# Optimization experiments

Hardware: AMD Instinct MI355X
Metric: run time of the kernel (lower is better)

## Reference

```python
import jax, jax.numpy as jnp
import numpy as np

B, T, D = 4, 1024, 1024
N_HEAD, HEAD, LATENT = 16, 64, 32
N_EXP, TOP_K, N_FF = 8, 2, 4096
HID = int(2 * N_FF / 3)  # 2730, Expert hidden when ffn_multiplier is None
CAP_FACTOR = 1.0


def setup_inputs() -> dict:
    key = jax.random.key(0)
    ks = jax.random.split(key, 14)
    s = 0.02
    f = lambda k, shp: jax.random.normal(k, shp, jnp.float32) * s
    return dict(
        x=jax.random.normal(ks[0], (B, T, D), jnp.float32),
        noise_eps=jax.random.normal(ks[1], (B, T, N_EXP), jnp.float32),
        ln1_w=jnp.ones((D,), jnp.float32),
        ln2_w=jnp.ones((D,), jnp.float32),
        q_w=f(ks[2], (N_HEAD, D, HEAD)), q_b=jnp.zeros((N_HEAD, HEAD), jnp.float32),
        ka_w=f(ks[3], (N_HEAD, D, LATENT)), kb_w=f(ks[4], (N_HEAD, LATENT, HEAD)),
        va_w=f(ks[5], (N_HEAD, D, LATENT)), vb_w=f(ks[6], (N_HEAD, LATENT, HEAD)),
        proj_w=f(ks[7], (D, D)), proj_b=jnp.zeros((D,), jnp.float32),
        route_w=f(ks[8], (D, N_EXP)), route_b=jnp.zeros((N_EXP,), jnp.float32),
        noise_w=f(ks[9], (D, N_EXP)), noise_b=jnp.zeros((N_EXP,), jnp.float32),
        swiglu_w=f(ks[10], (N_EXP, D, 2 * HID)),
        down_w=f(ks[11], (N_EXP, HID, D)),
    )


def _rms(x, w, eps=1e-5):
    x32 = x.astype(jnp.float32)
    n = x32 * jax.lax.rsqrt(jnp.mean(x32 * x32, -1, keepdims=True) + eps)
    return n.astype(x.dtype) * w


def _rope(q, k):
    # q,k: [B,H,T,hd]; even/odd split then concatenated halves (matches torch code)
    hd, Tq = q.shape[-1], q.shape[-2]
    inv = 1.0 / (10000.0 ** (jnp.arange(0, hd, 2, dtype=jnp.float32) / hd))
    ang = jnp.arange(Tq, dtype=jnp.float32)[:, None] * inv[None, :]  # [T, hd/2]
    cos, sin = jnp.cos(ang), jnp.sin(ang)
    def rot(t):
        t1, t2 = t[..., ::2], t[..., 1::2]
        return jnp.concatenate([t1 * cos - t2 * sin, t1 * sin + t2 * cos], -1)
    return rot(q), rot(k)


def reference(x, noise_eps, ln1_w, ln2_w, q_w, q_b, ka_w, kb_w, va_w, vb_w,
              proj_w, proj_b, route_w, route_b, noise_w, noise_b, swiglu_w, down_w):
    Bx, Tx, Dm = x.shape
    hd = q_w.shape[-1]
    E = route_w.shape[-1]
    # ---- Multi-Head Latent Attention (pre-norm) ----
    xn = _rms(x, ln1_w)
    q = jnp.einsum('btd,hde->bhte', xn, q_w) + q_b[None, :, None, :]
    k = jnp.einsum('bhtl,hle->bhte', jnp.einsum('btd,hdl->bhtl', xn, ka_w), kb_w)
    v = jnp.einsum('bhtl,hle->bhte', jnp.einsum('btd,hdl->bhtl', xn, va_w), vb_w)
    q, k = _rope(q, k)
    scores = jnp.einsum('bhtd,bhsd->bhts', q, k) / jnp.sqrt(jnp.float32(hd))
    attn = jax.nn.softmax(scores, axis=-1)  # NOTE: no causal mask in source
    o = jnp.einsum('bhts,bhsd->bhtd', attn, v)
    o = o.transpose(0, 2, 1, 3).reshape(Bx, Tx, Dm)
    x = x + (o @ proj_w + proj_b)
    # ---- Noisy top-k router ----
    xn2 = _rms(x, ln2_w)
    logits = xn2 @ route_w + route_b
    noisy = logits + noise_eps * jax.nn.softplus(xn2 @ noise_w + noise_b)  # temperature=1
    _, topi = jax.lax.top_k(noisy, TOP_K)  # [B,T,k]
    sel = jnp.any(jax.nn.one_hot(topi, E, dtype=jnp.bool_), axis=-2)  # [B,T,E]
    probs = jax.nn.softmax(jnp.where(sel, noisy, -jnp.inf), axis=-1)
    aux = jnp.sum((jnp.mean(probs, (0, 1)) - 1.0 / E) ** 2)
    # ---- Capacity-limited expert dispatch (first-come in flat token order) ----
    N = Bx * Tx
    cap = int(N * TOP_K / E * CAP_FACTOR)
    flat_x = xn2.reshape(N, Dm)
    flat_p = probs.reshape(N, E)
    flat_i = topi.reshape(N, TOP_K)
    upd = jnp.zeros((N, Dm), x.dtype)
    for e in range(E):
        m = jnp.any(flat_i == e, axis=-1)            # [N]
        pos = jnp.cumsum(m) - 1                      # slot within expert buffer
        keep = m & (pos < cap)
        slot = jnp.where(keep, pos, cap)             # dropped -> overflow slot
        tok = jnp.zeros(cap + 1, jnp.int32).at[slot].set(jnp.arange(N, dtype=jnp.int32))[:cap]
        valid = jnp.zeros(cap + 1, jnp.bool_).at[slot].set(keep)[:cap]
        xe = flat_x[tok] * valid[:, None]            # [cap, D]; zero rows yield zero output (no biases)
        h = xe @ swiglu_w[e]
        h1, h2 = jnp.split(h, 2, axis=-1)
        oe = (jax.nn.silu(h1) * h2) @ down_w[e]
        gate = jnp.where(valid, flat_p[tok, e], 0.0)
        upd = upd.at[tok].add(oe * gate[:, None])
    return x + upd.reshape(Bx, Tx, Dm), aux
```

## Files before the change

### kernel.cpp

```cpp
#include <hip/hip_runtime.h>
#include <math.h>

#define NTOK   4096
#define DM     1024
#define NHEAD  16
#define HDIM   64
#define NEXP   8
#define CAP    1024
#define HID    2730
#define NFF2   5460
#define HIDP   2752
#define KCD    86

typedef __attribute__((ext_vector_type(8))) short bf16x8;
typedef __attribute__((ext_vector_type(4))) float f32x4;
typedef __attribute__((ext_vector_type(8))) _Float16 h16x8;
typedef __attribute__((ext_vector_type(4))) _Float16 h16x4;
typedef __attribute__((ext_vector_type(8))) unsigned short u16x8;

__device__ __forceinline__ unsigned short f2bf(float f) {
  unsigned int u = __float_as_uint(f);
  u += 0x7fffu + ((u >> 16) & 1u);
  return (unsigned short)(u >> 16);
}

__global__ __launch_bounds__(256) void pack_dense3(const float* __restrict__ q_w,
                                                   const float* __restrict__ ka_w,
                                                   const float* __restrict__ va_w,
                                                   const float* __restrict__ proj_w,
                                                   unsigned short* __restrict__ Wqt,
                                                   unsigned short* __restrict__ Wlatt,
                                                   unsigned short* __restrict__ Wprojt) {
  int b = blockIdx.x;
  int tid = threadIdx.x;
  int col = tid & 63;
  int k0 = (tid >> 6) * 8;
  int which = b >> 9;
  int bb = b & 511;
  int nt = bb >> 5, kc = bb & 31;
  int d0 = kc * 32 + k0;
  u16x8 o;
  if (which == 0) {
    const float* src = q_w + ((size_t)nt * 1024 + d0) * 64 + col;
#pragma unroll
    for (int j = 0; j < 8; j++) o[j] = f2bf(src[(size_t)j * 64]);
    *(u16x8*)(Wqt + (size_t)bb * 2048 + col * 32 + k0) = o;
  } else if (which == 1) {
    int n = nt * 64 + col;
    const float* base;
    int h, l;
    if (n < 512) { h = n >> 5; l = n & 31; base = ka_w; }
    else { int m = n - 512; h = m >> 5; l = m & 31; base = va_w; }
    const float* src = base + ((size_t)h * 1024 + d0) * 32 + l;
#pragma unroll
    for (int j = 0; j < 8; j++) o[j] = f2bf(src[(size_t)j * 32]);
    *(u16x8*)(Wlatt + (size_t)bb * 2048 + col * 32 + k0) = o;
  } else {
    int n = nt * 64 + col;
    const float* src = proj_w + (size_t)d0 * 1024 + n;
#pragma unroll
    for (int j = 0; j < 8; j++) o[j] = f2bf(src[(size_t)j * 1024]);
    *(u16x8*)(Wprojt + (size_t)bb * 2048 + col * 32 + k0) = o;
  }
}

__global__ __launch_bounds__(256) void pack_swiglu(const float* __restrict__ swiglu_w,
                                                   unsigned short* __restrict__ Wpk) {
  int b = blockIdx.x;
  int kc32 = b & 31;
  int ejt = b >> 5;
  int jt = ejt % 43;
  int e = ejt / 43;
  int tid = threadIdx.x;
  int col = tid & 63;
  int k0 = (tid >> 6) * 8;
  int n = jt * 64 + col;
  bool nv = n < HID;
  const float* src = swiglu_w + ((size_t)e * DM + kc32 * 32 + k0) * NFF2 + n;
  u16x8 o1, o2;
#pragma unroll
  for (int j = 0; j < 8; j++) {
    float v1 = nv ? src[(size_t)j * NFF2] : 0.f;
    float v2 = nv ? src[(size_t)j * NFF2 + HID] : 0.f;
    o1[j] = f2bf(v1);
    o2[j] = f2bf(v2);
  }
  unsigned short* dst = Wpk + (size_t)b * 4096 + col * 32 + k0;
  *(u16x8*)dst = o1;
  *(u16x8*)(dst + 2048) = o2;
}

__global__ __launch_bounds__(256) void pack_down(const float* __restrict__ down_w,
                                                 unsigned short* __restrict__ Wdk) {
  int b = blockIdx.x;
  int kci = b % KCD;
  int ent = b / KCD;
  int nt = ent & 15;
  int e = ent >> 4;
  int tid = threadIdx.x;
  int col = tid & 63, k0 = (tid >> 6) * 8;
  int n = nt * 64 + col;
  int kbase = kci * 32 + k0;
  const float* src = down_w + ((size_t)e * HID + kbase) * DM + n;
  u16x8 o;
#pragma unroll
  for (int j = 0; j < 8; j++) {
    float v = (kbase + j < HID) ? src[(size_t)j * DM] : 0.f;
    o[j] = f2bf(v);
  }
  *(u16x8*)(Wdk + (size_t)b * 2048 + col * 32 + k0) = o;
}

template <bool F32OUT>
__global__ __launch_bounds__(256) void rms_kernel(const float* __restrict__ x,
                                                  const float* __restrict__ w,
                                                  float* __restrict__ out,
                                                  unsigned short* __restrict__ outb) {
  int row = blockIdx.x;
  int tid = threadIdx.x;
  const float4 v = ((const float4*)(x + (size_t)row * DM))[tid];
  float ss = v.x * v.x + v.y * v.y + v.z * v.z + v.w * v.w;
#pragma unroll
  for (int off = 32; off >= 1; off >>= 1) ss += __shfl_down(ss, off);
  __shared__ float red[4];
  if ((tid & 63) == 0) red[tid >> 6] = ss;
  __syncthreads();
  float tot = red[0] + red[1] + red[2] + red[3];
  float scale = rsqrtf(tot * (1.0f / 1024.0f) + 1e-5f);
  const float4 wv = ((const float4*)w)[tid];
  float4 o;
  o.x = v.x * scale * wv.x; o.y = v.y * scale * wv.y;
  o.z = v.z * scale * wv.z; o.w = v.w * scale * wv.w;
  if (F32OUT) ((float4*)(out + (size_t)row * DM))[tid] = o;
  ushort4 ob;
  ob.x = f2bf(o.x); ob.y = f2bf(o.y); ob.z = f2bf(o.z); ob.w = f2bf(o.w);
  *(ushort4*)(outb + (size_t)row * DM + tid * 4) = ob;
}

template <bool BIAS, bool RES>
__global__ __launch_bounds__(256) void mfma_dense(const unsigned short* __restrict__ A,
                                                  const unsigned short* __restrict__ Bpk,
                                                  const float* __restrict__ bias,
                                                  const float* __restrict__ res,
                                                  float* __restrict__ C, int K, int N) {
  int m0 = blockIdx.x * 128;
  int n0 = blockIdx.y * 128;
  int KC = K >> 5;
  __shared__ short As[128][40];
  __shared__ short Bs[128][40];
  int tid = threadIdx.x;
  int wid = tid >> 6, lane = tid & 63;
  int wm0 = (wid >> 1) * 64, wn0 = (wid & 1) * 64;
  int lr = lane & 15, lq = lane >> 4;
  f32x4 c[4][4];
  f32x4 zz = {0.f, 0.f, 0.f, 0.f};
#pragma unroll
  for (int i = 0; i < 4; i++)
#pragma unroll
    for (int j = 0; j < 4; j++) c[i][j] = zz;
  int ar = tid >> 2, aq = tid & 3;
  const unsigned short* Ap0 = A + (size_t)(m0 + ar) * K + aq * 8;
  const unsigned short* Ap1 = A + (size_t)(m0 + 64 + ar) * K + aq * 8;
  const unsigned short* Bt = Bpk + (size_t)(n0 >> 6) * KC * 2048 + tid * 8;
  u16x8 ra0 = *(const u16x8*)Ap0;
  u16x8 ra1 = *(const u16x8*)Ap1;
  u16x8 rb0 = *(const u16x8*)Bt;
  u16x8 rb1 = *(const u16x8*)(Bt + (size_t)KC * 2048);
  for (int kci = 0; kci < KC; kci++) {
    __syncthreads();
    *(u16x8*)&As[ar][aq * 8] = ra0;
    *(u16x8*)&As[64 + ar][aq * 8] = ra1;
    *(u16x8*)&Bs[tid >> 2][(tid & 3) * 8] = rb0;
    *(u16x8*)&Bs[64 + (tid >> 2)][(tid & 3) * 8] = rb1;
    __syncthreads();
    if (kci + 1 < KC) {
      ra0 = *(const u16x8*)(Ap0 + (kci + 1) * 32);
      ra1 = *(const u16x8*)(Ap1 + (kci + 1) * 32);
      rb0 = *(const u16x8*)(Bt + (size_t)(kci + 1) * 2048);
      rb1 = *(const u16x8*)(Bt + (size_t)(KC + kci + 1) * 2048);
    }
    bf16x8 a[4], b[4];
#pragma unroll
    for (int mi = 0; mi < 4; mi++) a[mi] = *(bf16x8*)&As[wm0 + mi * 16 + lr][lq * 8];
#pragma unroll
    for (int ni = 0; ni < 4; ni++) b[ni] = *(bf16x8*)&Bs[wn0 + ni * 16 + lr][lq * 8];
#pragma unroll
    for (int mi = 0; mi < 4; mi++)
#pragma unroll
      for (int ni = 0; ni < 4; ni++)
        c[mi][ni] = __builtin_amdgcn_mfma_f32_16x16x32_bf16(a[mi], b[ni], c[mi][ni], 0, 0, 0);
  }
#pragma unroll
  for (int mi = 0; mi < 4; mi++)
#pragma unroll
    for (int ni = 0; ni < 4; ni++) {
      int nn = n0 + wn0 + ni * 16 + lr;
      float bv = BIAS ? bias[nn] : 0.f;
#pragma unroll
      for (int r = 0; r < 4; r++) {
        int mm = m0 + wm0 + mi * 16 + lq * 4 + r;
        float v = c[mi][ni][r] + bv;
        if (RES) v += res[(size_t)mm * N + nn];
        C[(size_t)mm * N + nn] = v;
      }
    }
}

__global__ void expand_kernel(const float* __restrict__ latents, const float* __restrict__ kb_w,
                              const float* __restrict__ vb_w, float* __restrict__ kpre,
                              _Float16* __restrict__ vf) {
  int idx = blockIdx.x * 256 + threadIdx.x;
  int e = idx & 63;
  int t = (idx >> 6) & 1023;
  int h = (idx >> 16) & 15;
  int b = idx >> 20;
  const float* lrow = latents + ((size_t)(b * 1024 + t)) * DM;
  const float* kb = kb_w + (size_t)h * 2048;
  const float* vb = vb_w + (size_t)h * 2048;
  float ka = 0.f, va = 0.f;
#pragma unroll
  for (int l = 0; l < 32; l++) {
    ka += lrow[h * 32 + l] * kb[l * 64 + e];
    va += lrow[512 + h * 32 + l] * vb[l * 64 + e];
  }
  kpre[idx] = ka;
  vf[idx] = (_Float16)va;
}

template <bool IN_BTHD>
__global__ void rope_kernel(const float* __restrict__ in, _Float16* __restrict__ out) {
  int idx = blockIdx.x * 256 + threadIdx.x;
  int i = idx & 31;
  int t = (idx >> 5) & 1023;
  int h = (idx >> 15) & 15;
  int b = idx >> 19;
  size_t ib;
  if (IN_BTHD)
    ib = ((size_t)(b * 1024 + t)) * DM + h * 64;
  else
    ib = ((size_t)((b * 16 + h) * 1024 + t)) * 64;
  float t1 = in[ib + 2 * i], t2 = in[ib + 2 * i + 1];
  float inv = exp2f(-(float)i * 0.41524101186091903f);
  float ang = (float)t * inv;
  float s, c;
  sincosf(ang, &s, &c);
  size_t ob = ((size_t)((b * 16 + h) * 1024 + t)) * 64;
  out[ob + i] = (_Float16)(t1 * c - t2 * s);
  out[ob + 32 + i] = (_Float16)(t1 * s + t2 * c);
}

__global__ __launch_bounds__(256) void attn_mfma(const _Float16* __restrict__ qf,
                                                 const _Float16* __restrict__ kf,
                                                 const _Float16* __restrict__ vf,
                                                 unsigned short* __restrict__ o) {
  __shared__ _Float16 Ks[64][72];
  __shared__ _Float16 Vt[64][68];
  int bh = blockIdx.y;
  int q0 = blockIdx.x * 64;
  int tid = threadIdx.x;
  int wv = tid >> 6, lane = tid & 63;
  int lr = lane & 15, lq = lane >> 4;
  const size_t base = (size_t)bh * 1024 * 64;
  const _Float16* qrow = qf + base + (size_t)(q0 + wv * 16 + lr) * 64;
  h16x8 qfr[2];
  qfr[0] = *(const h16x8*)(qrow + lq * 8);
  qfr[1] = *(const h16x8*)(qrow + 32 + lq * 8);
  float mrow = -3.0e38f, lsum = 0.f;
  f32x4 oacc[4];
  f32x4 zz = {0.f, 0.f, 0.f, 0.f};
#pragma unroll
  for (int i = 0; i < 4; i++) oacc[i] = zz;
  int skey = tid >> 2, spart = tid & 3;
  int vkey = tid & 63, vdb = (tid >> 6) * 16;

// ... 95 lines not shown
    const float* nw = noise_w + d * 8;
#pragma unroll
    for (int e = 0; e < 8; e++) {
      acc[e] += xv * rw[e];
      nacc[e] += xv * nw[e];
    }
  }
#pragma unroll
  for (int off = 32; off >= 1; off >>= 1) {
#pragma unroll
    for (int e = 0; e < 8; e++) {
      acc[e] += __shfl_down(acc[e], off);
      nacc[e] += __shfl_down(nacc[e], off);
    }
  }
  if (lane == 0) {
    float noisy[8];
#pragma unroll
    for (int e = 0; e < 8; e++) {
      float lg = acc[e] + route_b[e];
      float nl = nacc[e] + noise_b[e];
      float sp = (nl > 20.f) ? nl : log1pf(expf(nl));
      noisy[e] = lg + noise_eps[tk * 8 + e] * sp;
    }
    int i1 = 0;
    float n1 = noisy[0];
#pragma unroll
    for (int e = 1; e < 8; e++)
      if (noisy[e] > n1) { n1 = noisy[e]; i1 = e; }
    int i2 = -1;
    float n2 = -3.0e38f;
#pragma unroll
    for (int e = 0; e < 8; e++)
      if (e != i1 && noisy[e] > n2) { n2 = noisy[e]; i2 = e; }
    float r = expf(n2 - n1);
    float p1 = 1.0f / (1.0f + r);
    float p2 = r / (1.0f + r);
    topi[tk * 2] = i1;
    topi[tk * 2 + 1] = i2;
#pragma unroll
    for (int e = 0; e < 8; e++) flat_p[tk * 8 + e] = (e == i1) ? p1 : ((e == i2) ? p2 : 0.f);
    atomicAdd(&probsum[i1], p1);
    atomicAdd(&probsum[i2], p2);
    slotmap[tk * 2] = -1;
    slotmap[tk * 2 + 1] = -1;
  }
}

__global__ __launch_bounds__(512) void scan_kernel(const int* __restrict__ topi,
                                                   const float* __restrict__ flat_p,
                                                   int* __restrict__ tok, float* __restrict__ gate,
                                                   int* __restrict__ cnt, int* __restrict__ slotmap) {
  int e = threadIdx.x >> 6;
  int lane = threadIdx.x & 63;
  int count = 0;
  for (int base = 0; base < NTOK; base += 64) {
    int t = base + lane;
    int a = topi[t * 2], b = topi[t * 2 + 1];
    bool mflag = (a == e) || (b == e);
    unsigned long long mask = __ballot(mflag);
    int pos = count + __popcll(mask & ((1ull << lane) - 1ull));
    if (mflag && pos < CAP) {
      tok[e * CAP + pos] = t;
      gate[e * CAP + pos] = flat_p[t * 8 + e];
      int k = (a == e) ? 0 : 1;
      slotmap[t * 2 + k] = pos;
    }
    count += __popcll(mask);
  }
  if (lane == 0) cnt[e] = (count < CAP) ? count : CAP;
}

__global__ __launch_bounds__(256) void mfma_swiglu(const unsigned short* __restrict__ xn2b,
                                                   const unsigned short* __restrict__ Wpk,
                                                   const int* __restrict__ tok,
                                                   const int* __restrict__ cnt,
                                                   unsigned short* __restrict__ ACT) {
  int L = blockIdx.x;
  int e = L & 7;
  int gw = L >> 3;
  int m0 = (gw & 7) * 128;
  int jt = gw >> 3;
  int j0 = jt * 64;
  __shared__ short As[128][40];
  __shared__ short B1s[64][40];
  __shared__ short B2s[64][40];
  __shared__ int tokL[128];
  int tid = threadIdx.x;
  if (tid < 128) {
    int slot = m0 + tid;
    tokL[tid] = (slot < cnt[e]) ? tok[e * CAP + slot] : 0;
  }
  __syncthreads();
  int wid = tid >> 6, lane = tid & 63;
  int wm0 = (wid >> 1) * 64, wn0 = (wid & 1) * 32;
  int lr = lane & 15, lq = lane >> 4;
  f32x4 c1[4][2], c2[4][2];
  f32x4 zz = {0.f, 0.f, 0.f, 0.f};
#pragma unroll
  for (int i = 0; i < 4; i++)
#pragma unroll
    for (int j = 0; j < 2; j++) { c1[i][j] = zz; c2[i][j] = zz; }
  int ar = tid >> 2, aq = tid & 3;
  const unsigned short* Ap0 = xn2b + (size_t)tokL[ar] * DM + aq * 8;
  const unsigned short* Ap1 = xn2b + (size_t)tokL[64 + ar] * DM + aq * 8;
  const unsigned short* wp = Wpk + (size_t)(e * 43 + jt) * 32 * 4096 + tid * 8;
  u16x8 ra0 = *(const u16x8*)Ap0;
  u16x8 ra1 = *(const u16x8*)Ap1;
  u16x8 rb1 = *(const u16x8*)wp;
  u16x8 rb2 = *(const u16x8*)(wp + 2048);

  for (int kci = 0; kci < 32; kci++) {
    __syncthreads();
    *(u16x8*)&As[ar][aq * 8] = ra0;
    *(u16x8*)&As[64 + ar][aq * 8] = ra1;
    *(u16x8*)&B1s[tid >> 2][(tid & 3) * 8] = rb1;
    *(u16x8*)&B2s[tid >> 2][(tid & 3) * 8] = rb2;
    __syncthreads();
    if (kci < 31) {
      ra0 = *(const u16x8*)(Ap0 + (kci + 1) * 32);
      ra1 = *(const u16x8*)(Ap1 + (kci + 1) * 32);
      rb1 = *(const u16x8*)(wp + (size_t)(kci + 1) * 4096);
      rb2 = *(const u16x8*)(wp + (size_t)(kci + 1) * 4096 + 2048);
    }
    bf16x8 a[4], b1[2], b2[2];
#pragma unroll
    for (int mi = 0; mi < 4; mi++) a[mi] = *(bf16x8*)&As[wm0 + mi * 16 + lr][lq * 8];
#pragma unroll
    for (int ni = 0; ni < 2; ni++) {
      b1[ni] = *(bf16x8*)&B1s[wn0 + ni * 16 + lr][lq * 8];
      b2[ni] = *(bf16x8*)&B2s[wn0 + ni * 16 + lr][lq * 8];
    }
#pragma unroll
    for (int mi = 0; mi < 4; mi++)
#pragma unroll
      for (int ni = 0; ni < 2; ni++) {
        c1[mi][ni] = __builtin_amdgcn_mfma_f32_16x16x32_bf16(a[mi], b1[ni], c1[mi][ni], 0, 0, 0);
        c2[mi][ni] = __builtin_amdgcn_mfma_f32_16x16x32_bf16(a[mi], b2[ni], c2[mi][ni], 0, 0, 0);
      }
  }
#pragma unroll
  for (int mi = 0; mi < 4; mi++)
#pragma unroll
    for (int ni = 0; ni < 2; ni++)
#pragma unroll
      for (int r = 0; r < 4; r++) {
        int mm = m0 + wm0 + mi * 16 + lq * 4 + r;
        int cc = j0 + wn0 + ni * 16 + lr;
        float h1 = c1[mi][ni][r], h2 = c2[mi][ni][r];
        float act = (h1 / (1.0f + expf(-h1))) * h2;
        ACT[(size_t)e * CAP * HIDP + (size_t)mm * HIDP + cc] = f2bf(act);
      }
}

__global__ __launch_bounds__(256) void mfma_down(const unsigned short* __restrict__ ACT,
                                                 const unsigned short* __restrict__ Wdk,
                                                 float* __restrict__ OE) {
  int L = blockIdx.x;
  int e = L & 7;
  int gw = L >> 3;
  int m0 = (gw & 7) * 128;
  int nt0 = (gw >> 3) * 2;
  int n0 = nt0 * 64;
  __shared__ short As[128][40];
  __shared__ short Bs[128][40];
  int tid = threadIdx.x;
  int wid = tid >> 6, lane = tid & 63;
  int wm0 = (wid >> 1) * 64, wn0 = (wid & 1) * 64;
  int lr = lane & 15, lq = lane >> 4;
  f32x4 c[4][4];
  f32x4 zz = {0.f, 0.f, 0.f, 0.f};
#pragma unroll
  for (int i = 0; i < 4; i++)
#pragma unroll
    for (int j = 0; j < 4; j++) c[i][j] = zz;
  int ar = tid >> 2, aq = tid & 3;
  const unsigned short* Ab = ACT + (size_t)e * CAP * HIDP + (size_t)m0 * HIDP;
  const unsigned short* Ap0 = Ab + (size_t)ar * HIDP + aq * 8;
  const unsigned short* Ap1 = Ab + (size_t)(64 + ar) * HIDP + aq * 8;
  const unsigned short* Bt = Wdk + (size_t)(e * 16 + nt0) * KCD * 2048 + tid * 8;
  u16x8 ra0 = *(const u16x8*)Ap0;
  u16x8 ra1 = *(const u16x8*)Ap1;
  u16x8 rb0 = *(const u16x8*)Bt;
  u16x8 rb1 = *(const u16x8*)(Bt + (size_t)KCD * 2048);

  for (int kci = 0; kci < KCD; kci++) {
    __syncthreads();
    *(u16x8*)&As[ar][aq * 8] = ra0;
    *(u16x8*)&As[64 + ar][aq * 8] = ra1;
    *(u16x8*)&Bs[tid >> 2][(tid & 3) * 8] = rb0;
    *(u16x8*)&Bs[64 + (tid >> 2)][(tid & 3) * 8] = rb1;
    __syncthreads();
    if (kci + 1 < KCD) {
      ra0 = *(const u16x8*)(Ap0 + (kci + 1) * 32);
      ra1 = *(const u16x8*)(Ap1 + (kci + 1) * 32);
      rb0 = *(const u16x8*)(Bt + (size_t)(kci + 1) * 2048);
      rb1 = *(const u16x8*)(Bt + (size_t)(KCD + kci + 1) * 2048);
    }
    bf16x8 a[4], b[4];
#pragma unroll
    for (int mi = 0; mi < 4; mi++) a[mi] = *(bf16x8*)&As[wm0 + mi * 16 + lr][lq * 8];
#pragma unroll
    for (int ni = 0; ni < 4; ni++) b[ni] = *(bf16x8*)&Bs[wn0 + ni * 16 + lr][lq * 8];
#pragma unroll
    for (int mi = 0; mi < 4; mi++)
#pragma unroll
      for (int ni = 0; ni < 4; ni++)
        c[mi][ni] = __builtin_amdgcn_mfma_f32_16x16x32_bf16(a[mi], b[ni], c[mi][ni], 0, 0, 0);
  }
#pragma unroll
  for (int mi = 0; mi < 4; mi++)
#pragma unroll
    for (int ni = 0; ni < 4; ni++)
#pragma unroll
      for (int r = 0; r < 4; r++) {
        int mm = m0 + wm0 + mi * 16 + lq * 4 + r;
        int nn = n0 + wn0 + ni * 16 + lr;
        OE[((size_t)e << 20) + (size_t)mm * DM + nn] = c[mi][ni][r];
      }
}

__global__ void combine_kernel(const float* __restrict__ x2, const float* __restrict__ OE,
                               const int* __restrict__ topi, const int* __restrict__ slotmap,
                               const float* __restrict__ flat_p, float* __restrict__ out) {
  int idx = blockIdx.x * 256 + threadIdx.x;
  int t = idx >> 8;
  int c4 = (idx & 255) * 4;
  float4 v = *(const float4*)(x2 + (size_t)t * DM + c4);
#pragma unroll
  for (int k = 0; k < 2; k++) {
    int s = slotmap[t * 2 + k];
    if (s >= 0) {
      int e = topi[t * 2 + k];
      float g = flat_p[t * 8 + e];
      float4 ov = *(const float4*)(OE + ((size_t)e << 20) + (size_t)s * DM + c4);
      v.x += g * ov.x; v.y += g * ov.y; v.z += g * ov.z; v.w += g * ov.w;
    }
  }
  *(float4*)(out + (size_t)t * DM + c4) = v;
}

__global__ void aux_kernel(const float* __restrict__ probsum, float* __restrict__ out) {
  if (threadIdx.x == 0) {
    float s = 0.f;
#pragma unroll
    for (int e = 0; e < 8; e++) {
      float d = probsum[e] * (1.0f / 4096.0f) - 0.125f;
      s += d * d;
    }
    out[4194304] = s;
  }
}

extern "C" void kernel_launch(void* const* d_in, const int* in_sizes, int n_in, void* d_out,
                              int out_size, void* d_ws, size_t ws_size, hipStream_t stream) {
  const float* x = (const float*)d_in[0];
  const float* noise_eps = (const float*)d_in[1];
  const float* ln1_w = (const float*)d_in[2];
  const float* ln2_w = (const float*)d_in[3];
  const float* q_w = (const float*)d_in[4];
  const float* q_b = (const float*)d_in[5];
  const float* ka_w = (const float*)d_in[6];
  const float* kb_w = (const float*)d_in[7];
  const float* va_w = (const float*)d_in[8];
  const float* vb_w = (const float*)d_in[9];
  const float* proj_w = (const float*)d_in[10];
  const float* proj_b = (const float*)d_in[11];
  const float* route_w = (const float*)d_in[12];
  const float* route_b = (const float*)d_in[13];
  const float* noise_w = (const float*)d_in[14];
  const float* noise_b = (const float*)d_in[15];
  const float* swiglu_w = (const float*)d_in[16];
  const float* down_w = (const float*)d_in[17];
  float* out = (float*)d_out;
  char* w = (char*)d_ws;
  const size_t MB = 1ull << 20;

  float* x2 = (float*)(w + 0 * MB);
  float* xn2 = (float*)(w + 16 * MB);
  unsigned short* xn2b = (unsigned short*)(w + 32 * MB);
  char* sm = w + 40 * MB;
  unsigned short* xnb = (unsigned short*)(w + 42 * MB);
  float* qtmp = (float*)(w + 50 * MB);
  float* latents = (float*)(w + 66 * MB);
  float* kpre = (float*)(w + 82 * MB);
  _Float16* qfb = (_Float16*)(w + 98 * MB);
  _Float16* kfb = (_Float16*)(w + 106 * MB);
  _Float16* vfb = (_Float16*)(w + 114 * MB);
  unsigned short* obb = (unsigned short*)(w + 122 * MB);
  unsigned short* Wqt = (unsigned short*)(w + 130 * MB);
  unsigned short* Wlatt = (unsigned short*)(w + 132 * MB);
  unsigned short* Wprojt = (unsigned short*)(w + 134 * MB);
// ... 35 lines not shown
```

Before: 942.3 us.

## Process two K-chunks per barrier and remap weight pack/LDS store layout

Measured after the change: 923.3 us. -2.0%, faster.

```diff
diff --git a/kernel.cpp b/kernel.cpp
--- a/kernel.cpp
+++ b/kernel.cpp
@@ -44,7 +44,7 @@
     const float* src = q_w + ((size_t)nt * 1024 + d0) * 64 + col;
 #pragma unroll
     for (int j = 0; j < 8; j++) o[j] = f2bf(src[(size_t)j * 64]);
-    *(u16x8*)(Wqt + (size_t)bb * 2048 + col * 32 + k0) = o;
+    *(u16x8*)(Wqt + (size_t)bb * 2048 + tid * 8) = o;
   } else if (which == 1) {
     int n = nt * 64 + col;
     const float* base;
@@ -54,13 +54,13 @@
     const float* src = base + ((size_t)h * 1024 + d0) * 32 + l;
 #pragma unroll
     for (int j = 0; j < 8; j++) o[j] = f2bf(src[(size_t)j * 32]);
-    *(u16x8*)(Wlatt + (size_t)bb * 2048 + col * 32 + k0) = o;
+    *(u16x8*)(Wlatt + (size_t)bb * 2048 + tid * 8) = o;
   } else {
     int n = nt * 64 + col;
     const float* src = proj_w + (size_t)d0 * 1024 + n;
 #pragma unroll
     for (int j = 0; j < 8; j++) o[j] = f2bf(src[(size_t)j * 1024]);
-    *(u16x8*)(Wprojt + (size_t)bb * 2048 + col * 32 + k0) = o;
+    *(u16x8*)(Wprojt + (size_t)bb * 2048 + tid * 8) = o;
   }
 }
 
@@ -85,7 +85,7 @@
     o1[j] = f2bf(v1);
     o2[j] = f2bf(v2);
   }
-  unsigned short* dst = Wpk + (size_t)b * 4096 + col * 32 + k0;
+  unsigned short* dst = Wpk + (size_t)b * 4096 + tid * 8;
   *(u16x8*)dst = o1;
   *(u16x8*)(dst + 2048) = o2;
 }
@@ -108,7 +108,7 @@
     float v = (kbase + j < HID) ? src[(size_t)j * DM] : 0.f;
     o[j] = f2bf(v);
   }
-  *(u16x8*)(Wdk + (size_t)b * 2048 + col * 32 + k0) = o;
+  *(u16x8*)(Wdk + (size_t)b * 2048 + tid * 8) = o;
 }
 
 template <bool F32OUT>
@@ -146,50 +146,61 @@
   int m0 = blockIdx.x * 128;
   int n0 = blockIdx.y * 128;
   int KC = K >> 5;
-  __shared__ short As[128][40];
-  __shared__ short Bs[128][40];
+  int KK = KC >> 1;
+  __shared__ short As[2][128][40];
+  __shared__ short Bs[2][128][40];
   int tid = threadIdx.x;
-  int wid = tid >> 6, lane = tid & 63;
+  int l6 = tid & 63, wid = tid >> 6;
+  int lr = l6 & 15, lq = l6 >> 4;
   int wm0 = (wid >> 1) * 64, wn0 = (wid & 1) * 64;
-  int lr = lane & 15, lq = lane >> 4;
   f32x4 c[4][4];
   f32x4 zz = {0.f, 0.f, 0.f, 0.f};
 #pragma unroll
   for (int i = 0; i < 4; i++)
 #pragma unroll
     for (int j = 0; j < 4; j++) c[i][j] = zz;
-  int ar = tid >> 2, aq = tid & 3;
-  const unsigned short* Ap0 = A + (size_t)(m0 + ar) * K + aq * 8;
-  const unsigned short* Ap1 = A + (size_t)(m0 + 64 + ar) * K + aq * 8;
+  const unsigned short* Ap0 = A + (size_t)(m0 + l6) * K + wid * 8;
+  const unsigned short* Ap1 = A + (size_t)(m0 + 64 + l6) * K + wid * 8;
   const unsigned short* Bt = Bpk + (size_t)(n0 >> 6) * KC * 2048 + tid * 8;
-  u16x8 ra0 = *(const u16x8*)Ap0;
-  u16x8 ra1 = *(const u16x8*)Ap1;
-  u16x8 rb0 = *(const u16x8*)Bt;
-  u16x8 rb1 = *(const u16x8*)(Bt + (size_t)KC * 2048);
-  for (int kci = 0; kci < KC; kci++) {
+  u16x8 ra0[2], ra1[2], rb0[2], rb1[2];
+#define DEN_LOAD(kk)                                                        \
+  {                                                                         \
+    ra0[0] = *(const u16x8*)(Ap0 + (kk) * 64);                              \
+    ra0[1] = *(const u16x8*)(Ap0 + (kk) * 64 + 32);                         \
+    ra1[0] = *(const u16x8*)(Ap1 + (kk) * 64);                              \
+    ra1[1] = *(const u16x8*)(Ap1 + (kk) * 64 + 32);                         \
+    rb0[0] = *(const u16x8*)(Bt + (size_t)(2 * (kk)) * 2048);               \
+    rb0[1] = *(const u16x8*)(Bt + (size_t)(2 * (kk) + 1) * 2048);           \
+    rb1[0] = *(const u16x8*)(Bt + (size_t)(KC + 2 * (kk)) * 2048);          \
+    rb1[1] = *(const u16x8*)(Bt + (size_t)(KC + 2 * (kk) + 1) * 2048);      \
+  }
+  DEN_LOAD(0);
+  for (int kk = 0; kk < KK; kk++) {
     __syncthreads();
-    *(u16x8*)&As[ar][aq * 8] = ra0;
-    *(u16x8*)&As[64 + ar][aq * 8] = ra1;
-    *(u16x8*)&Bs[tid >> 2][(tid & 3) * 8] = rb0;
-    *(u16x8*)&Bs[64 + (tid >> 2)][(tid & 3) * 8] = rb1;
+#pragma unroll
+    for (int p = 0; p < 2; p++) {
+      *(u16x8*)&As[p][l6][wid * 8] = ra0[p];
+      *(u16x8*)&As[p][64 + l6][wid * 8] = ra1[p];
+      *(u16x8*)&Bs[p][l6][wid * 8] = rb0[p];
+      *(u16x8*)&Bs[p][64 + l6][wid * 8] = rb1[p];
+    }
     __syncthreads();
-    if (kci + 1 < KC) {
-      ra0 = *(const u16x8*)(Ap0 + (kci + 1) * 32);
-      ra1 = *(const u16x8*)(Ap1 + (kci + 1) * 32);
-      rb0 = *(const u16x8*)(Bt + (size_t)(kci + 1) * 2048);
-      rb1 = *(const u16x8*)(Bt + (size_t)(KC + kci + 1) * 2048);
-    }
-    bf16x8 a[4], b[4];
-#pragma unroll
-    for (int mi = 0; mi < 4; mi++) a[mi] = *(bf16x8*)&As[wm0 + mi * 16 + lr][lq * 8];
-#pragma unroll
-    for (int ni = 0; ni < 4; ni++) b[ni] = *(bf16x8*)&Bs[wn0 + ni * 16 + lr][lq * 8];
-#pragma unroll
-    for (int mi = 0; mi < 4; mi++)
-#pragma unroll
-      for (int ni = 0; ni < 4; ni++)
-        c[mi][ni] = __builtin_amdgcn_mfma_f32_16x16x32_bf16(a[mi], b[ni], c[mi][ni], 0, 0, 0);
-  }
+    if (kk + 1 < KK) { DEN_LOAD(kk + 1); }
+#pragma unroll
+    for (int p = 0; p < 2; p++) {
+      bf16x8 a[4], b[4];
+#pragma unroll
+      for (int mi = 0; mi < 4; mi++) a[mi] = *(bf16x8*)&As[p][wm0 + mi * 16 + lr][lq * 8];
+#pragma unroll
+      for (int ni = 0; ni < 4; ni++) b[ni] = *(bf16x8*)&Bs[p][wn0 + ni * 16 + lr][lq * 8];
+#pragma unroll
+      for (int mi = 0; mi < 4; mi++)
+#pragma unroll
+        for (int ni = 0; ni < 4; ni++)
+          c[mi][ni] = __builtin_amdgcn_mfma_f32_16x16x32_bf16(a[mi], b[ni], c[mi][ni], 0, 0, 0);
+    }
+  }
+#undef DEN_LOAD
 #pragma unroll
   for (int mi = 0; mi < 4; mi++)
 #pragma unroll
@@ -451,63 +462,70 @@
   int m0 = (gw & 7) * 128;
   int jt = gw >> 3;
   int j0 = jt * 64;
-  __shared__ short As[128][40];
-  __shared__ short B1s[64][40];
-  __shared__ short B2s[64][40];
-  __shared__ int tokL[128];
+  __shared__ short As[2][128][40];
+  __shared__ short B1s[2][64][40];
+  __shared__ short B2s[2][64][40];
   int tid = threadIdx.x;
-  if (tid < 128) {
-    int slot = m0 + tid;
-    tokL[tid] = (slot < cnt[e]) ? tok[e * CAP + slot] : 0;
-  }
-  __syncthreads();
-  int wid = tid >> 6, lane = tid & 63;
+  int l6 = tid & 63, wid = tid >> 6;
+  int lr = l6 & 15, lq = l6 >> 4;
   int wm0 = (wid >> 1) * 64, wn0 = (wid & 1) * 32;
-  int lr = lane & 15, lq = lane >> 4;
+  int ce = cnt[e];
+  int s0 = m0 + l6, s1 = s0 + 64;
+  int tr0 = (s0 < ce) ? tok[e * CAP + s0] : 0;
+  int tr1 = (s1 < ce) ? tok[e * CAP + s1] : 0;
+  const unsigned short* Ap0 = xn2b + (size_t)tr0 * DM + wid * 8;
+  const unsigned short* Ap1 = xn2b + (size_t)tr1 * DM + wid * 8;
+  const unsigned short* wp = Wpk + (size_t)(e * 43 + jt) * 32 * 4096 + tid * 8;
   f32x4 c1[4][2], c2[4][2];
   f32x4 zz = {0.f, 0.f, 0.f, 0.f};
 #pragma unroll
   for (int i = 0; i < 4; i++)
 #pragma unroll
     for (int j = 0; j < 2; j++) { c1[i][j] = zz; c2[i][j] = zz; }
-  int ar = tid >> 2, aq = tid & 3;
-  const unsigned short* Ap0 = xn2b + (size_t)tokL[ar] * DM + aq * 8;
-  const unsigned short* Ap1 = xn2b + (size_t)tokL[64 + ar] * DM + aq * 8;
-  const unsigned short* wp = Wpk + (size_t)(e * 43 + jt) * 32 * 4096 + tid * 8;
-  u16x8 ra0 = *(const u16x8*)Ap0;
-  u16x8 ra1 = *(const u16x8*)Ap1;
-  u16x8 rb1 = *(const u16x8*)wp;
-  u16x8 rb2 = *(const u16x8*)(wp + 2048);
-
-  for (int kci = 0; kci < 32; kci++) {
+  u16x8 ra0[2], ra1[2], rbl[2], rbr[2];
+#define SWG_LOAD(kk)                                                          \
+  {                                                                           \
+    ra0[0] = *(const u16x8*)(Ap0 + (kk) * 64);                                \
+    ra0[1] = *(const u16x8*)(Ap0 + (kk) * 64 + 32);                           \
+    ra1[0] = *(const u16x8*)(Ap1 + (kk) * 64);                                \
+    ra1[1] = *(const u16x8*)(Ap1 + (kk) * 64 + 32);                           \
+    rbl[0] = *(const u16x8*)(wp + (size_t)(2 * (kk)) * 4096);                 \
+    rbr[0] = *(const u16x8*)(wp + (size_t)(2 * (kk)) * 4096 + 2048);          \
+    rbl[1] = *(const u16x8*)(wp + (size_t)(2 * (kk) + 1) * 4096);             \
+    rbr[1] = *(const u16x8*)(wp + (size_t)(2 * (kk) + 1) * 4096 + 2048);      \
+  }
+  SWG_LOAD(0);
+  for (int kk = 0; kk < 16; kk++) {
     __syncthreads();
-    *(u16x8*)&As[ar][aq * 8] = ra0;
-    *(u16x8*)&As[64 + ar][aq * 8] = ra1;
-    *(u16x8*)&B1s[tid >> 2][(tid & 3) * 8] = rb1;
-    *(u16x8*)&B2s[tid >> 2][(tid & 3) * 8] = rb2;
+#pragma unroll
+    for (int p = 0; p < 2; p++) {
+      *(u16x8*)&As[p][l6][wid * 8] = ra0[p];
+      *(u16x8*)&As[p][64 + l6][wid * 8] = ra1[p];
+      *(u16x8*)&B1s[p][l6][wid * 8] = rbl[p];
+      *(u16x8*)&B2s[p][l6][wid * 8] = rbr[p];
+    }
     __syncthreads();
-    if (kci < 31) {
-      ra0 = *(const u16x8*)(Ap0 + (kci + 1) * 32);
-      ra1 = *(const u16x8*)(Ap1 + (kci + 1) * 32);
-      rb1 = *(const u16x8*)(wp + (size_t)(kci + 1) * 4096);
-      rb2 = *(const u16x8*)(wp + (size_t)(kci + 1) * 4096 + 2048);
-    }
-    bf16x8 a[4], b1[2], b2[2];
-#pragma unroll
-    for (int mi = 0; mi < 4; mi++) a[mi] = *(bf16x8*)&As[wm0 + mi * 16 + lr][lq * 8];
-#pragma unroll
-    for (int ni = 0; ni < 2; ni++) {
-      b1[ni] = *(bf16x8*)&B1s[wn0 + ni * 16 + lr][lq * 8];
-      b2[ni] = *(bf16x8*)&B2s[wn0 + ni * 16 + lr][lq * 8];
-    }
-#pragma unroll
-    for (int mi = 0; mi < 4; mi++)
+    if (kk < 15) { SWG_LOAD(kk + 1); }
+#pragma unroll
+    for (int p = 0; p < 2; p++) {
+      bf16x8 a[4], b1[2], b2[2];
+#pragma unroll
+      for (int mi = 0; mi < 4; mi++) a[mi] = *(bf16x8*)&As[p][wm0 + mi * 16 + lr][lq * 8];
 #pragma unroll
       for (int ni = 0; ni < 2; ni++) {
-        c1[mi][ni] = __builtin_amdgcn_mfma_f32_16x16x32_bf16(a[mi], b1[ni], c1[mi][ni], 0, 0, 0);
-        c2[mi][ni] = __builtin_amdgcn_mfma_f32_16x16x32_bf16(a[mi], b2[ni], c2[mi][ni], 0, 0, 0);
-      }
-  }
+        b1[ni] = *(bf16x8*)&B1s[p][wn0 + ni * 16 + lr][lq * 8];
+        b2[ni] = *(bf16x8*)&B2s[p][wn0 + ni * 16 + lr][lq * 8];
+      }
+#pragma unroll
+      for (int mi = 0; mi < 4; mi++)
+#pragma unroll
+        for (int ni = 0; ni < 2; ni++) {
+          c1[mi][ni] = __builtin_amdgcn_mfma_f32_16x16x32_bf16(a[mi], b1[ni], c1[mi][ni], 0, 0, 0);
+          c2[mi][ni] = __builtin_amdgcn_mfma_f32_16x16x32_bf16(a[mi], b2[ni], c2[mi][ni], 0, 0, 0);
+        }
+    }
+  }
+#undef SWG_LOAD
 #pragma unroll
   for (int mi = 0; mi < 4; mi++)
 #pragma unroll
@@ -531,52 +549,61 @@
   int m0 = (gw & 7) * 128;
   int nt0 = (gw >> 3) * 2;
   int n0 = nt0 * 64;
-  __shared__ short As[128][40];
-  __shared__ short Bs[128][40];
+  __shared__ short As[2][128][40];
+  __shared__ short Bs[2][128][40];
   int tid = threadIdx.x;
-  int wid = tid >> 6, lane = tid & 63;
+  int l6 = tid & 63, wid = tid >> 6;
+  int lr = l6 & 15, lq = l6 >> 4;
   int wm0 = (wid >> 1) * 64, wn0 = (wid & 1) * 64;
-  int lr = lane & 15, lq = lane >> 4;
   f32x4 c[4][4];
   f32x4 zz = {0.f, 0.f, 0.f, 0.f};
 #pragma unroll
   for (int i = 0; i < 4; i++)
 #pragma unroll
     for (int j = 0; j < 4; j++) c[i][j] = zz;
-  int ar = tid >> 2, aq = tid & 3;
   const unsigned short* Ab = ACT + (size_t)e * CAP * HIDP + (size_t)m0 * HIDP;
-  const unsigned short* Ap0 = Ab + (size_t)ar * HIDP + aq * 8;
-  const unsigned short* Ap1 = Ab + (size_t)(64 + ar) * HIDP + aq * 8;
+  const unsigned short* Ap0 = Ab + (size_t)l6 * HIDP + wid * 8;
+  const unsigned short* Ap1 = Ab + (size_t)(64 + l6) * HIDP + wid * 8;
   const unsigned short* Bt = Wdk + (size_t)(e * 16 + nt0) * KCD * 2048 + tid * 8;
-  u16x8 ra0 = *(const u16x8*)Ap0;
-  u16x8 ra1 = *(const u16x8*)Ap1;
-  u16x8 rb0 = *(const u16x8*)Bt;
-  u16x8 rb1 = *(const u16x8*)(Bt + (size_t)KCD * 2048);
-
-  for (int kci = 0; kci < KCD; kci++) {
+  u16x8 ra0[2], ra1[2], rb0[2], rb1[2];
+#define DWN_LOAD(kk)                                                          \
+  {                                                                           \
+    ra0[0] = *(const u16x8*)(Ap0 + (kk) * 64);                                \
+    ra0[1] = *(const u16x8*)(Ap0 + (kk) * 64 + 32);                           \
+    ra1[0] = *(const u16x8*)(Ap1 + (kk) * 64);                                \
+    ra1[1] = *(const u16x8*)(Ap1 + (kk) * 64 + 32);                           \
+    rb0[0] = *(const u16x8*)(Bt + (size_t)(2 * (kk)) * 2048);                 \
+    rb0[1] = *(const u16x8*)(Bt + (size_t)(2 * (kk) + 1) * 2048);             \
+    rb1[0] = *(const u16x8*)(Bt + (size_t)(KCD + 2 * (kk)) * 2048);           \
+    rb1[1] = *(const u16x8*)(Bt + (size_t)(KCD + 2 * (kk) + 1) * 2048);       \
+  }
+  DWN_LOAD(0);
+  for (int kk = 0; kk < 43; kk++) {
     __syncthreads();
-    *(u16x8*)&As[ar][aq * 8] = ra0;
-    *(u16x8*)&As[64 + ar][aq * 8] = ra1;
-    *(u16x8*)&Bs[tid >> 2][(tid & 3) * 8] = rb0;
-    *(u16x8*)&Bs[64 + (tid >> 2)][(tid & 3) * 8] = rb1;
+#pragma unroll
+    for (int p = 0; p < 2; p++) {
+      *(u16x8*)&As[p][l6][wid * 8] = ra0[p];
+      *(u16x8*)&As[p][64 + l6][wid * 8] = ra1[p];
+      *(u16x8*)&Bs[p][l6][wid * 8] = rb0[p];
+      *(u16x8*)&Bs[p][64 + l6][wid * 8] = rb1[p];
+    }
     __syncthreads();
-    if (kci + 1 < KCD) {
-      ra0 = *(const u16x8*)(Ap0 + (kci + 1) * 32);
-      ra1 = *(const u16x8*)(Ap1 + (kci + 1) * 32);
-      rb0 = *(const u16x8*)(Bt + (size_t)(kci + 1) * 2048);
-      rb1 = *(const u16x8*)(Bt + (size_t)(KCD + kci + 1) * 2048);
-    }
-    bf16x8 a[4], b[4];
-#pragma unroll
-    for (int mi = 0; mi < 4; mi++) a[mi] = *(bf16x8*)&As[wm0 + mi * 16 + lr][lq * 8];
-#pragma unroll
-    for (int ni = 0; ni < 4; ni++) b[ni] = *(bf16x8*)&Bs[wn0 + ni * 16 + lr][lq * 8];
-#pragma unroll
-    for (int mi = 0; mi < 4; mi++)
-#pragma unroll
-      for (int ni = 0; ni < 4; ni++)
-        c[mi][ni] = __builtin_amdgcn_mfma_f32_16x16x32_bf16(a[mi], b[ni], c[mi][ni], 0, 0, 0);
-  }
+    if (kk < 42) { DWN_LOAD(kk + 1); }
+#pragma unroll
+    for (int p = 0; p < 2; p++) {
+      bf16x8 a[4], b[4];
+#pragma unroll
+      for (int mi = 0; mi < 4; mi++) a[mi] = *(bf16x8*)&As[p][wm0 + mi * 16 + lr][lq * 8];
+#pragma unroll
+      for (int ni = 0; ni < 4; ni++) b[ni] = *(bf16x8*)&Bs[p][wn0 + ni * 16 + lr][lq * 8];
+#pragma unroll
+      for (int mi = 0; mi < 4; mi++)
+#pragma unroll
+        for (int ni = 0; ni < 4; ni++)
+          c[mi][ni] = __builtin_amdgcn_mfma_f32_16x16x32_bf16(a[mi], b[ni], c[mi][ni], 0, 0, 0);
+    }
+  }
+#undef DWN_LOAD
 #pragma unroll
   for (int mi = 0; mi < 4; mi++)
 #pragma unroll
```

## Use direct global-to-LDS loads with double-buffered shared tiles in GEMMs

Applied to the files above, without the earlier changes.

Result: slower. 966.2 us (+2.5%).

```diff
diff --git a/kernel.cpp b/kernel.cpp
--- a/kernel.cpp
+++ b/kernel.cpp
@@ -24,6 +24,11 @@
   return (unsigned short)(u >> 16);
 }
 
+__device__ __forceinline__ void gll16(const void* g, void* l) {
+  __builtin_amdgcn_global_load_lds((const __attribute__((address_space(1))) void*)g,
+                                   (__attribute__((address_space(3))) void*)l, 16, 0, 0);
+}
+
 __global__ __launch_bounds__(256) void pack_dense3(const float* __restrict__ q_w,
                                                    const float* __restrict__ ka_w,
                                                    const float* __restrict__ va_w,
@@ -44,7 +49,7 @@
     const float* src = q_w + ((size_t)nt * 1024 + d0) * 64 + col;
 #pragma unroll
     for (int j = 0; j < 8; j++) o[j] = f2bf(src[(size_t)j * 64]);
-    *(u16x8*)(Wqt + (size_t)bb * 2048 + col * 32 + k0) = o;
+    *(u16x8*)(Wqt + (size_t)bb * 2048 + tid * 8) = o;
   } else if (which == 1) {
     int n = nt * 64 + col;
     const float* base;
@@ -54,13 +59,13 @@
     const float* src = base + ((size_t)h * 1024 + d0) * 32 + l;
 #pragma unroll
     for (int j = 0; j < 8; j++) o[j] = f2bf(src[(size_t)j * 32]);
-    *(u16x8*)(Wlatt + (size_t)bb * 2048 + col * 32 + k0) = o;
+    *(u16x8*)(Wlatt + (size_t)bb * 2048 + tid * 8) = o;
   } else {
     int n = nt * 64 + col;
     const float* src = proj_w + (size_t)d0 * 1024 + n;
 #pragma unroll
     for (int j = 0; j < 8; j++) o[j] = f2bf(src[(size_t)j * 1024]);
-    *(u16x8*)(Wprojt + (size_t)bb * 2048 + col * 32 + k0) = o;
+    *(u16x8*)(Wprojt + (size_t)bb * 2048 + tid * 8) = o;
   }
 }
 
@@ -85,7 +90,7 @@
     o1[j] = f2bf(v1);
     o2[j] = f2bf(v2);
   }
-  unsigned short* dst = Wpk + (size_t)b * 4096 + col * 32 + k0;
+  unsigned short* dst = Wpk + (size_t)b * 4096 + tid * 8;
   *(u16x8*)dst = o1;
   *(u16x8*)(dst + 2048) = o2;
 }
@@ -108,7 +113,7 @@
     float v = (kbase + j < HID) ? src[(size_t)j * DM] : 0.f;
     o[j] = f2bf(v);
   }
-  *(u16x8*)(Wdk + (size_t)b * 2048 + col * 32 + k0) = o;
+  *(u16x8*)(Wdk + (size_t)b * 2048 + tid * 8) = o;
 }
 
 template <bool F32OUT>
@@ -146,50 +151,49 @@
   int m0 = blockIdx.x * 128;
   int n0 = blockIdx.y * 128;
   int KC = K >> 5;
-  __shared__ short As[128][40];
-  __shared__ short Bs[128][40];
-  int tid = threadIdx.x;
-  int wid = tid >> 6, lane = tid & 63;
+  __shared__ unsigned short Asl[2][4096];
+  __shared__ unsigned short Bsl[2][4096];
+  int tid = threadIdx.x;
+  int l6 = tid & 63, wid = tid >> 6;
+  int lr = l6 & 15, lq = l6 >> 4;
   int wm0 = (wid >> 1) * 64, wn0 = (wid & 1) * 64;
-  int lr = lane & 15, lq = lane >> 4;
+  int aw = wid * 512;
   f32x4 c[4][4];
   f32x4 zz = {0.f, 0.f, 0.f, 0.f};
 #pragma unroll
   for (int i = 0; i < 4; i++)
 #pragma unroll
     for (int j = 0; j < 4; j++) c[i][j] = zz;
-  int ar = tid >> 2, aq = tid & 3;
-  const unsigned short* Ap0 = A + (size_t)(m0 + ar) * K + aq * 8;
-  const unsigned short* Ap1 = A + (size_t)(m0 + 64 + ar) * K + aq * 8;
-  const unsigned short* Bt = Bpk + (size_t)(n0 >> 6) * KC * 2048 + tid * 8;
-  u16x8 ra0 = *(const u16x8*)Ap0;
-  u16x8 ra1 = *(const u16x8*)Ap1;
-  u16x8 rb0 = *(const u16x8*)Bt;
-  u16x8 rb1 = *(const u16x8*)(Bt + (size_t)KC * 2048);
+  const unsigned short* aAg = A + (size_t)(m0 + (tid & 127)) * K + (tid >> 7) * 8;
+  const unsigned short* bg0 = Bpk + (size_t)((n0 >> 6) * KC) * 2048 + tid * 8;
+  const unsigned short* bg1 = Bpk + (size_t)(((n0 >> 6) + 1) * KC) * 2048 + tid * 8;
+#define DEN_STG(cur, kci)                                       \
+  {                                                             \
+    gll16(aAg + (kci) * 32, &Asl[cur][aw]);                     \
+    gll16(aAg + (kci) * 32 + 16, &Asl[cur][2048 + aw]);         \
+    gll16(bg0 + (size_t)(kci) * 2048, &Bsl[cur][aw]);           \
+    gll16(bg1 + (size_t)(kci) * 2048, &Bsl[cur][2048 + aw]);    \
+  }
+  DEN_STG(0, 0);
+  __syncthreads();
   for (int kci = 0; kci < KC; kci++) {
-    __syncthreads();
-    *(u16x8*)&As[ar][aq * 8] = ra0;
-    *(u16x8*)&As[64 + ar][aq * 8] = ra1;
-    *(u16x8*)&Bs[tid >> 2][(tid & 3) * 8] = rb0;
-    *(u16x8*)&Bs[64 + (tid >> 2)][(tid & 3) * 8] = rb1;
-    __syncthreads();
-    if (kci + 1 < KC) {
-      ra0 = *(const u16x8*)(Ap0 + (kci + 1) * 32);
-      ra1 = *(const u16x8*)(Ap1 + (kci + 1) * 32);
-      rb0 = *(const u16x8*)(Bt + (size_t)(kci + 1) * 2048);
-      rb1 = *(const u16x8*)(Bt + (size_t)(KC + kci + 1) * 2048);
-    }
+    int cur = kci & 1;
+    if (kci + 1 < KC) DEN_STG(cur ^ 1, kci + 1);
     bf16x8 a[4], b[4];
 #pragma unroll
-    for (int mi = 0; mi < 4; mi++) a[mi] = *(bf16x8*)&As[wm0 + mi * 16 + lr][lq * 8];
-#pragma unroll
-    for (int ni = 0; ni < 4; ni++) b[ni] = *(bf16x8*)&Bs[wn0 + ni * 16 + lr][lq * 8];
+    for (int mi = 0; mi < 4; mi++)
+      a[mi] = *(bf16x8*)&Asl[cur][(lq * 128 + wm0 + mi * 16 + lr) * 8];
+#pragma unroll
+    for (int ni = 0; ni < 4; ni++)
+      b[ni] = *(bf16x8*)&Bsl[cur][((wn0 >> 6) * 256 + lq * 64 + ni * 16 + lr) * 8];
 #pragma unroll
     for (int mi = 0; mi < 4; mi++)
 #pragma unroll
       for (int ni = 0; ni < 4; ni++)
         c[mi][ni] = __builtin_amdgcn_mfma_f32_16x16x32_bf16(a[mi], b[ni], c[mi][ni], 0, 0, 0);
-  }
+    __syncthreads();
+  }
+#undef DEN_STG
 #pragma unroll
   for (int mi = 0; mi < 4; mi++)
 #pragma unroll
@@ -451,54 +455,45 @@
   int m0 = (gw & 7) * 128;
   int jt = gw >> 3;
   int j0 = jt * 64;
-  __shared__ short As[128][40];
-  __shared__ short B1s[64][40];
-  __shared__ short B2s[64][40];
-  __shared__ int tokL[128];
-  int tid = threadIdx.x;
-  if (tid < 128) {
-    int slot = m0 + tid;
-    tokL[tid] = (slot < cnt[e]) ? tok[e * CAP + slot] : 0;
-  }
-  __syncthreads();
-  int wid = tid >> 6, lane = tid & 63;
+  __shared__ unsigned short Asl[2][4096];
+  __shared__ unsigned short B1sl[2][2048];
+  __shared__ unsigned short B2sl[2][2048];
+  int tid = threadIdx.x;
+  int l6 = tid & 63, wid = tid >> 6;
+  int lr = l6 & 15, lq = l6 >> 4;
   int wm0 = (wid >> 1) * 64, wn0 = (wid & 1) * 32;
-  int lr = lane & 15, lq = lane >> 4;
+  int aw = wid * 512;
+  int ce = cnt[e];
+  int slot = m0 + (tid & 127);
+  int tr = (slot < ce) ? tok[e * CAP + slot] : 0;
+  const unsigned short* aAg = xn2b + (size_t)tr * DM + (tid >> 7) * 8;
+  const unsigned short* wg = Wpk + (size_t)(e * 43 + jt) * 32 * 4096 + tid * 8;
   f32x4 c1[4][2], c2[4][2];
   f32x4 zz = {0.f, 0.f, 0.f, 0.f};
 #pragma unroll
   for (int i = 0; i < 4; i++)
 #pragma unroll
     for (int j = 0; j < 2; j++) { c1[i][j] = zz; c2[i][j] = zz; }
-  int ar = tid >> 2, aq = tid & 3;
-  const unsigned short* Ap0 = xn2b + (size_t)tokL[ar] * DM + aq * 8;
-  const unsigned short* Ap1 = xn2b + (size_t)tokL[64 + ar] * DM + aq * 8;
-  const unsigned short* wp = Wpk + (size_t)(e * 43 + jt) * 32 * 4096 + tid * 8;
-  u16x8 ra0 = *(const u16x8*)Ap0;
-  u16x8 ra1 = *(const u16x8*)Ap1;
-  u16x8 rb1 = *(const u16x8*)wp;
-  u16x8 rb2 = *(const u16x8*)(wp + 2048);
-
+#define SWG_STG(cur, kci)                                        \
+  {                                                              \
+    gll16(aAg + (kci) * 32, &Asl[cur][aw]);                      \
+    gll16(aAg + (kci) * 32 + 16, &Asl[cur][2048 + aw]);          \
+    gll16(wg + (size_t)(kci) * 4096, &B1sl[cur][aw]);            \
+    gll16(wg + (size_t)(kci) * 4096 + 2048, &B2sl[cur][aw]);     \
+  }
+  SWG_STG(0, 0);
+  __syncthreads();
   for (int kci = 0; kci < 32; kci++) {
-    __syncthreads();
-    *(u16x8*)&As[ar][aq * 8] = ra0;
-    *(u16x8*)&As[64 + ar][aq * 8] = ra1;
-    *(u16x8*)&B1s[tid >> 2][(tid & 3) * 8] = rb1;
-    *(u16x8*)&B2s[tid >> 2][(tid & 3) * 8] = rb2;
-    __syncthreads();
-    if (kci < 31) {
-      ra0 = *(const u16x8*)(Ap0 + (kci + 1) * 32);
-      ra1 = *(const u16x8*)(Ap1 + (kci + 1) * 32);
-      rb1 = *(const u16x8*)(wp + (size_t)(kci + 1) * 4096);
-      rb2 = *(const u16x8*)(wp + (size_t)(kci + 1) * 4096 + 2048);
-    }
+    int cur = kci & 1;
+    if (kci + 1 < 32) SWG_STG(cur ^ 1, kci + 1);
     bf16x8 a[4], b1[2], b2[2];
 #pragma unroll
-    for (int mi = 0; mi < 4; mi++) a[mi] = *(bf16x8*)&As[wm0 + mi * 16 + lr][lq * 8];
+    for (int mi = 0; mi < 4; mi++)
+      a[mi] = *(bf16x8*)&Asl[cur][(lq * 128 + wm0 + mi * 16 + lr) * 8];
 #pragma unroll
     for (int ni = 0; ni < 2; ni++) {
-      b1[ni] = *(bf16x8*)&B1s[wn0 + ni * 16 + lr][lq * 8];
-      b2[ni] = *(bf16x8*)&B2s[wn0 + ni * 16 + lr][lq * 8];
+      b1[ni] = *(bf16x8*)&B1sl[cur][(lq * 64 + wn0 + ni * 16 + lr) * 8];
+      b2[ni] = *(bf16x8*)&B2sl[cur][(lq * 64 + wn0 + ni * 16 + lr) * 8];
     }
 #pragma unroll
     for (int mi = 0; mi < 4; mi++)
@@ -507,7 +502,9 @@
         c1[mi][ni] = __builtin_amdgcn_mfma_f32_16x16x32_bf16(a[mi], b1[ni], c1[mi][ni], 0, 0, 0);
         c2[mi][ni] = __builtin_amdgcn_mfma_f32_16x16x32_bf16(a[mi], b2[ni], c2[mi][ni], 0, 0, 0);
       }
-  }
+    __syncthreads();
+  }
+#undef SWG_STG
 #pragma unroll
   for (int mi = 0; mi < 4; mi++)
 #pragma unroll
@@ -531,52 +528,50 @@
   int m0 = (gw & 7) * 128;
   int nt0 = (gw >> 3) * 2;
   int n0 = nt0 * 64;
-  __shared__ short As[128][40];
-  __shared__ short Bs[128][40];
-  int tid = threadIdx.x;
-  int wid = tid >> 6, lane = tid & 63;
+  __shared__ unsigned short Asl[2][4096];
+  __shared__ unsigned short Bsl[2][4096];
+  int tid = threadIdx.x;
+  int l6 = tid & 63, wid = tid >> 6;
+  int lr = l6 & 15, lq = l6 >> 4;
   int wm0 = (wid >> 1) * 64, wn0 = (wid & 1) * 64;
-  int lr = lane & 15, lq = lane >> 4;
+  int aw = wid * 512;
   f32x4 c[4][4];
   f32x4 zz = {0.f, 0.f, 0.f, 0.f};
 #pragma unroll
   for (int i = 0; i < 4; i++)
 #pragma unroll
     for (int j = 0; j < 4; j++) c[i][j] = zz;
-  int ar = tid >> 2, aq = tid & 3;
-  const unsigned short* Ab = ACT + (size_t)e * CAP * HIDP + (size_t)m0 * HIDP;
-  const unsigned short* Ap0 = Ab + (size_t)ar * HIDP + aq * 8;
-  const unsigned short* Ap1 = Ab + (size_t)(64 + ar) * HIDP + aq * 8;
-  const unsigned short* Bt = Wdk + (size_t)(e * 16 + nt0) * KCD * 2048 + tid * 8;
-  u16x8 ra0 = *(const u16x8*)Ap0;
-  u16x8 ra1 = *(const u16x8*)Ap1;
-  u16x8 rb0 = *(const u16x8*)Bt;
-  u16x8 rb1 = *(const u16x8*)(Bt + (size_t)KCD * 2048);
-
+  const unsigned short* aAg =
+      ACT + (size_t)e * CAP * HIDP + (size_t)(m0 + (tid & 127)) * HIDP + (tid >> 7) * 8;
+  const unsigned short* bg0 = Wdk + ((size_t)(e * 16 + nt0) * KCD) * 2048 + tid * 8;
+  const unsigned short* bg1 = Wdk + ((size_t)(e * 16 + nt0 + 1) * KCD) * 2048 + tid * 8;
+#define DWN_STG(cur, kci)                                       \
+  {                                                             \
+    gll16(aAg + (kci) * 32, &Asl[cur][aw]);                     \
+    gll16(aAg + (kci) * 32 + 16, &Asl[cur][2048 + aw]);         \
+    gll16(bg0 + (size_t)(kci) * 2048, &Bsl[cur][aw]);           \
+    gll16(bg1 + (size_t)(kci) * 2048, &Bsl[cur][2048 + aw]);    \
+  }
+  DWN_STG(0, 0);
+  __syncthreads();
   for (int kci = 0; kci < KCD; kci++) {
-    __syncthreads();
-    *(u16x8*)&As[ar][aq * 8] = ra0;
-    *(u16x8*)&As[64 + ar][aq * 8] = ra1;
-    *(u16x8*)&Bs[tid >> 2][(tid & 3) * 8] = rb0;
-    *(u16x8*)&Bs[64 + (tid >> 2)][(tid & 3) * 8] = rb1;
-    __syncthreads();
-    if (kci + 1 < KCD) {
-      ra0 = *(const u16x8*)(Ap0 + (kci + 1) * 32);
-      ra1 = *(const u16x8*)(Ap1 + (kci + 1) * 32);
-      rb0 = *(const u16x8*)(Bt + (size_t)(kci + 1) * 2048);
-      rb1 = *(const u16x8*)(Bt + (size_t)(KCD + kci + 1) * 2048);
-    }
+    int cur = kci & 1;
+    if (kci + 1 < KCD) DWN_STG(cur ^ 1, kci + 1);
     bf16x8 a[4], b[4];
 #pragma unroll
-    for (int mi = 0; mi < 4; mi++) a[mi] = *(bf16x8*)&As[wm0 + mi * 16 + lr][lq * 8];
-#pragma unroll
-    for (int ni = 0; ni < 4; ni++) b[ni] = *(bf16x8*)&Bs[wn0 + ni * 16 + lr][lq * 8];
+    for (int mi = 0; mi < 4; mi++)
+      a[mi] = *(bf16x8*)&Asl[cur][(lq * 128 + wm0 + mi * 16 + lr) * 8];
+#pragma unroll
+    for (int ni = 0; ni < 4; ni++)
+      b[ni] = *(bf16x8*)&Bsl[cur][((wn0 >> 6) * 256 + lq * 64 + ni * 16 + lr) * 8];
 #pragma unroll
     for (int mi = 0; mi < 4; mi++)
 #pragma unroll
       for (int ni = 0; ni < 4; ni++)
         c[mi][ni] = __builtin_amdgcn_mfma_f32_16x16x32_bf16(a[mi], b[ni], c[mi][ni], 0, 0, 0);
-  }
+    __syncthreads();
+  }
+#undef DWN_STG
 #pragma unroll
   for (int mi = 0; mi < 4; mi++)
 #pragma unroll
```
